# Performance work log

Hardware: AMD Instinct MI355X
Metric: run time of the kernel (lower is better)

## Reference

```python
import jax, jax.numpy as jnp
import numpy as np

D_MODEL = 768
D_LATENT = 12288
K = 20
N = 16384


def setup_inputs() -> dict:
    key = jax.random.key(0)
    k1, k2, k3, k4, k5 = jax.random.split(key, 5)
    x = jax.random.normal(k1, (N, D_MODEL), dtype=jnp.float32)
    # nn.Linear default init scale ~ 1/sqrt(fan_in)
    W_enc = jax.random.normal(k2, (D_LATENT, D_MODEL), dtype=jnp.float32) / np.sqrt(D_MODEL)
    b_enc = jax.random.normal(k3, (D_LATENT,), dtype=jnp.float32) * 0.01
    W_dec = jax.random.normal(k4, (D_MODEL, D_LATENT), dtype=jnp.float32) / np.sqrt(D_LATENT)
    b_dec = jax.random.normal(k5, (D_MODEL,), dtype=jnp.float32) * 0.01
    return {"x": x, "W_enc": W_enc, "b_enc": b_enc, "W_dec": W_dec, "b_dec": b_dec}


def reference(x, W_enc, b_enc, W_dec, b_dec):
    # encode: [N, 12288]
    latents = jnp.einsum('nd,ld->nl', x, W_enc) + b_enc
    # top-k(20) per row; scatter kept values back into zeros == latents * mask
    vals, idx = jax.lax.top_k(latents, K)            # [N, K]
    rows = jnp.arange(latents.shape[0])[:, None]      # [N, 1]
    sparse = jnp.zeros_like(latents).at[rows, idx].set(vals)
    # decode: [N, 768]
    recons = jnp.einsum('nl,dl->nd', sparse, W_dec) + b_dec
    return recons
```

## Files before the change

### kernel.cpp

```cpp
#include <hip/hip_runtime.h>
#include <hip/hip_bf16.h>
#include <stdint.h>

#define D_MODEL_  768
#define D_LATENT_ 12288
#define N_ROWS_   16384
#define TOPK_     20
#define TOPC      16
#define NQ        8
#define NC        128
#define NREF      28
#define THR0      1.7f

#define BM 256
#define BN 128
#define BK 64
#define KT (D_MODEL_ / BK)
#define CTQ (D_LATENT_ / NQ / BN)
#define NTHREADS 1024
#define CAP 8

#define BUFSZ 49152

typedef float f4 __attribute__((ext_vector_type(4)));
typedef short bf16x8 __attribute__((ext_vector_type(8)));

typedef const void __attribute__((address_space(1)))* gptr_t;
typedef void __attribute__((address_space(3)))* lptr_t;

__device__ __forceinline__ void stage16(const void* g, void* l) {
  __builtin_amdgcn_global_load_lds((gptr_t)g, (lptr_t)l, 16, 0, 0);
}

__device__ __forceinline__ unsigned short bf16_rne(float f) {
  unsigned u = __builtin_bit_cast(unsigned, f);
  u += 0x7FFFu + ((u >> 16) & 1u);
  return (unsigned short)(u >> 16);
}
__device__ __forceinline__ float bf16_to_f(unsigned short h) {
  return __builtin_bit_cast(float, ((unsigned)h) << 16);
}

#define BAR_LGKM() do { asm volatile("s_waitcnt lgkmcnt(0)" ::: "memory"); \
                        __builtin_amdgcn_s_barrier(); } while (0)

__global__ void tobf16_kernel(const float4* __restrict__ in, ushort4* __restrict__ o, int n4) {
  int i = blockIdx.x * blockDim.x + threadIdx.x;
  if (i >= n4) return;
  float4 v = in[i];
  ushort4 h;
  h.x = bf16_rne(v.x); h.y = bf16_rne(v.y); h.z = bf16_rne(v.z); h.w = bf16_rne(v.w);
  o[i] = h;
}

__global__ void transpose_bf16_kernel(const float* __restrict__ wd, unsigned short* __restrict__ wdT) {
  __shared__ float tile[32][33];
  const int l0 = blockIdx.x * 32;
  const int d0 = blockIdx.y * 32;
  const int tx = threadIdx.x, ty = threadIdx.y;
#pragma unroll
  for (int i = 0; i < 32; i += 8)
    tile[ty + i][tx] = wd[(size_t)(d0 + ty + i) * D_LATENT_ + l0 + tx];
  __syncthreads();
#pragma unroll
  for (int i = 0; i < 32; i += 8)
    wdT[(size_t)(l0 + ty + i) * D_MODEL_ + d0 + tx] = bf16_rne(tile[tx][ty + i]);
}

__global__ __launch_bounds__(NTHREADS, 4) void sae_topk(
    const unsigned short* __restrict__ xh, const unsigned short* __restrict__ wh,
    const float* __restrict__ b_enc, unsigned* __restrict__ candp)
{
  __shared__ __align__(16) unsigned char smem[2 * BUFSZ];
  __shared__ float s_topv[BM][TOPC];
  __shared__ int   s_topi[BM][TOPC];
  __shared__ float s_candv[BM][CAP];
  __shared__ int   s_candi[BM][CAP];
  __shared__ float s_thr[BM];
  __shared__ int   s_cnt[BM];
  __shared__ int   s_flag;

  const int tid  = threadIdx.x;
  const int lane = tid & 63;
  const int wid  = tid >> 6;
  const int wm   = wid >> 2;
  const int wn   = wid & 3;
  const int quar = blockIdx.x & 7;
  const int brow = (blockIdx.x >> 3) * BM;
  const int cbase = quar * (D_LATENT_ / NQ);

  auto stage_tile = [&](int buf, int ct, int kt) {
    unsigned char* base = smem + buf * BUFSZ;
#pragma unroll
    for (int j = 0; j < 2; ++j) {
      const int cid = tid + j * 1024;
      const int row = cid >> 3, slot = cid & 7;
      stage16(xh + (size_t)(brow + row) * D_MODEL_ + kt * BK + (slot ^ (row & 7)) * 8,
              base + cid * 16);
    }
    {
      const int row = tid >> 3, slot = tid & 7;
      stage16(wh + (size_t)(cbase + ct * BN + row) * D_MODEL_ + kt * BK + (slot ^ (row & 7)) * 8,
              base + 32768 + tid * 16);
    }
  };

  stage_tile(0, 0, 0);

  if (tid < BM) { s_thr[tid] = THR0; s_cnt[tid] = 0; }
  if (tid == 0) s_flag = 0;
  for (int i = tid; i < BM * TOPC; i += NTHREADS) {
    (&s_topv[0][0])[i] = -__builtin_inff();
    (&s_topi[0][0])[i] = 0;
  }

  f4 acc[4][2];
#pragma unroll
  for (int m = 0; m < 4; ++m)
#pragma unroll
    for (int n = 0; n < 2; ++n) { f4 z = {0.f, 0.f, 0.f, 0.f}; acc[m][n] = z; }

  int cur = 0;
#pragma unroll 1
  for (int ct = 0; ct < CTQ; ++ct) {
    const float be0 = b_enc[cbase + ct * BN + wn * 32 + (lane & 15)];
    const float be1 = b_enc[cbase + ct * BN + wn * 32 + 16 + (lane & 15)];

#pragma unroll 1
    for (int kt = 0; kt < KT; ++kt) {
      bool more = true;
      if (kt < KT - 1)       stage_tile(cur ^ 1, ct, kt + 1);
      else if (ct + 1 < CTQ) stage_tile(cur ^ 1, ct + 1, 0);
      else                   more = false;
      if (more) { asm volatile("s_waitcnt vmcnt(3)" ::: "memory"); }
      else      { asm volatile("s_waitcnt vmcnt(0)" ::: "memory"); }
      __builtin_amdgcn_s_barrier();
      {
        const unsigned char* base = smem + cur * BUFSZ;
#pragma unroll
        for (int ks = 0; ks < 2; ++ks) {
          const int c = ks * 4 + (lane >> 4);
          bf16x8 ah[4], bh[2];
#pragma unroll
          for (int m = 0; m < 4; ++m) {
            const int row = wm * 64 + m * 16 + (lane & 15);
            ah[m] = *(const bf16x8*)(base + row * 128 + ((c ^ (row & 7)) << 4));
          }
#pragma unroll
          for (int n = 0; n < 2; ++n) {
            const int col = wn * 32 + n * 16 + (lane & 15);
            bh[n] = *(const bf16x8*)(base + 32768 + col * 128 + ((c ^ (col & 7)) << 4));
          }
#pragma unroll
          for (int m = 0; m < 4; ++m)
#pragma unroll
            for (int n = 0; n < 2; ++n)
              acc[m][n] = __builtin_amdgcn_mfma_f32_16x16x32_bf16(ah[m], bh[n], acc[m][n], 0, 0, 0);
        }
      }
      __builtin_amdgcn_s_barrier();
      cur ^= 1;
    }

#pragma unroll
    for (int m = 0; m < 4; ++m) {
      acc[m][0][0] += be0; acc[m][0][1] += be0; acc[m][0][2] += be0; acc[m][0][3] += be0;
      acc[m][1][0] += be1; acc[m][1][1] += be1; acc[m][1][2] += be1; acc[m][1][3] += be1;
    }

    unsigned pend = ~0u;
#pragma unroll 1
    for (;;) {
#pragma unroll
      for (int m = 0; m < 4; ++m)
#pragma unroll
        for (int n = 0; n < 2; ++n)
#pragma unroll
          for (int j = 0; j < 4; ++j) {
            const int b = m * 8 + n * 4 + j;
            if (pend & (1u << b)) {
              const int row = wm * 64 + m * 16 + ((lane >> 4) << 2) + j;
              const float v = acc[m][n][j];
              if (v <= s_thr[row]) {
                pend &= ~(1u << b);
              } else {
                const int pos = atomicAdd(&s_cnt[row], 1);
                if (pos < CAP) {
                  s_candv[row][pos] = v;
                  s_candi[row][pos] = cbase + ct * BN + wn * 32 + n * 16 + (lane & 15);
                  pend &= ~(1u << b);
                }
              }
            }
          }
      BAR_LGKM();
      if (tid < BM) {
        const int row = tid;
        const int nc = s_cnt[row];
        if (nc > 0) {
          if (nc > CAP) s_flag = 1;
          float minv = s_topv[row][0]; int minp = 0;
#pragma unroll
          for (int k = 1; k < TOPC; ++k) { const float t = s_topv[row][k]; if (t < minv) { minv = t; minp = k; } }
          const int ne = nc < CAP ? nc : CAP;
          for (int j = 0; j < ne; ++j) {
            const float v = s_candv[row][j];
            if (v > minv) {
              s_topv[row][minp] = v; s_topi[row][minp] = s_candi[row][j];
              minv = s_topv[row][0]; minp = 0;
#pragma unroll
              for (int k = 1; k < TOPC; ++k) { const float t = s_topv[row][k]; if (t < minv) { minv = t; minp = k; } }
            }
          }
          s_thr[row] = minv > THR0 ? minv : THR0;
          s_cnt[row] = 0;
        }
      }
      BAR_LGKM();
      const int f = s_flag;
      BAR_LGKM();
      if (!f) break;
      if (tid == 0) s_flag = 0;
    }

#pragma unroll
    for (int m = 0; m < 4; ++m)
#pragma unroll
      for (int n = 0; n < 2; ++n) { f4 z = {0.f, 0.f, 0.f, 0.f}; acc[m][n] = z; }
  }

  if (tid < BM) {
#pragma unroll
    for (int k = 0; k < TOPC; ++k) {
      const float v = s_topv[tid][k];
      unsigned p = 0u;
      if (v > 0.f) p = ((unsigned)bf16_rne(v) << 16) | (unsigned)s_topi[tid][k];
      candp[(size_t)(brow + tid) * NC + quar * TOPC + k] = p;
    }
  }
}

__device__ __forceinline__ float chunk_fma(const float* __restrict__ xr,
                                           const float* __restrict__ wr,
                                           int beg, int end) {
  float a = 0.f;
#pragma unroll 4
  for (int d0 = beg; d0 < end; d0 += 4) {
    const float4 xv = *(const float4*)(xr + d0);
    const float4 wv = *(const float4*)(wr + d0);
    a = fmaf(xv.x, wv.x, a);
    a = fmaf(xv.y, wv.y, a);
    a = fmaf(xv.z, wv.z, a);
    a = fmaf(xv.w, wv.w, a);
  }
  return a;
}

__global__ __launch_bounds__(256) void refine_decode11(
    const float* __restrict__ x, const float* __restrict__ W_enc,
    const float* __restrict__ b_enc, const unsigned* __restrict__ candp,
    const unsigned short* __restrict__ wdTb, const float* __restrict__ b_dec,
    float* __restrict__ out)
{
  __shared__ unsigned s_p[4][NC];
  __shared__ unsigned s_ref[4][NREF];
  __shared__ float s_rv[4][NREF];
  __shared__ int   s_rid[4][NREF];
  __shared__ float s_selv[4][TOPK_];
  __shared__ int   s_seli[4][TOPK_];

  const int tid  = threadIdx.x;
  const int w    = tid >> 6;
  const int lane = tid & 63;
  const int row  = blockIdx.x * 4 + w;

  s_p[w][lane]      = candp[(size_t)row * NC + lane];
  s_p[w][lane + 64] = candp[(size_t)row * NC + lane + 64];
  __syncthreads();

#pragma unroll
  for (int t = 0; t < 2; ++t) {
    const int i = lane + t * 64;
    const unsigned p = s_p[w][i];
    int r = 0;
#pragma unroll 1
    for (int j = 0; j < NC; ++j) r += (s_p[w][j] > p);
    if (r < NREF && p != 0u) s_ref[w][r] = p;
  }
  __syncthreads();

  if (lane < NREF) {
    const unsigned p = s_ref[w][lane];
    const int idx = (int)(p & 0x3FFFu);
    const float* xr = x + (size_t)row * D_MODEL_;
    const float* wr = W_enc + (size_t)idx * D_MODEL_;
    const float a1 = chunk_fma(xr, wr, 0, 320);
    const float a2 = chunk_fma(xr, wr, 320, 544);
    const float a3 = chunk_fma(xr, wr, 544, 768);
    s_rv[w][lane]  = ((a1 + a2) + a3) + b_enc[idx];
    s_rid[w][lane] = idx;
  }
  __syncthreads();

  if (lane < NREF) {
    const float v = s_rv[w][lane]; const int id = s_rid[w][lane];
    int rank = 0;
#pragma unroll 1
    for (int j = 0; j < NREF; ++j) {
      const float vj = s_rv[w][j];
      rank += (vj > v) || (vj == v && s_rid[w][j] > id);
    }
    if (rank < TOPK_) { s_selv[w][rank] = v; s_seli[w][rank] = id; }
  }
  __syncthreads();

#pragma unroll 1
  for (int r = 0; r < 4; ++r) {
#pragma unroll
    for (int j = 0; j < 3; ++j) {
      const int d = tid + j * 256;
      float a = b_dec[d];
#pragma unroll
      for (int k = 0; k < TOPK_; ++k)
        a = fmaf(s_selv[r][k], bf16_to_f(wdTb[(size_t)s_seli[r][k] * D_MODEL_ + d]), a);
      out[(size_t)(blockIdx.x * 4 + r) * D_MODEL_ + d] = a;
    }
  }
}

extern "C" void kernel_launch(void* const* d_in, const int* in_sizes, int n_in,
                              void* d_out, int out_size, void* d_ws, size_t ws_size,
                              hipStream_t stream) {
  const float* x     = (const float*)d_in[0];
  const float* W_enc = (const float*)d_in[1];
  const float* b_enc = (const float*)d_in[2];
  const float* W_dec = (const float*)d_in[3];
  const float* b_dec = (const float*)d_in[4];
  float* out = (float*)d_out;
  char* ws = (char*)d_ws;

  unsigned short* xh = (unsigned short*)(ws + 0);
  unsigned short* wh = (unsigned short*)(ws + 25165824);
  unsigned*     candp = (unsigned*)(ws + 44040192);
  unsigned short* wdTb = (unsigned short*)(ws + 0);

  {
    int n4 = N_ROWS_ * D_MODEL_ / 4;
    tobf16_kernel<<<(n4 + 255) / 256, 256, 0, stream>>>((const float4*)x, (ushort4*)xh, n4);
  }
  {
    int n4 = D_LATENT_ * D_MODEL_ / 4;
    tobf16_kernel<<<(n4 + 255) / 256, 256, 0, stream>>>((const float4*)W_enc, (ushort4*)wh, n4);
  }

  sae_topk<<<(N_ROWS_ / BM) * NQ, NTHREADS, 0, stream>>>(xh, wh, b_enc, candp);

  transpose_bf16_kernel<<<dim3(D_LATENT_ / 32, D_MODEL_ / 32), dim3(32, 8), 0, stream>>>(W_dec, wdTb);

  refine_decode11<<<N_ROWS_ / 4, 256, 0, stream>>>(x, W_enc, b_enc, candp, wdTb, b_dec, out);
}
```

Baseline: 929.4 us.

## Widen encoder tile to 256 columns, pack top-k entries, auto-accept top candidates

The encoder GEMM tile grows from 128 to 256 latent columns per step. Each warp now holds a 4x4 set of MFMA accumulators, and the LDS buffers are enlarged to match, raising operand reuse per staged A tile. The per-row top-16 tracking now stores packed bf16-value/index words instead of separate float and int arrays, which cuts shared-memory traffic in the merge. The refine kernel accepts the 12 highest bf16 candidates without recomputing them and recomputes exactly in fp32 only the next 16 to fill the remaining 8 slots, reducing refine FMAs. The risk is that ranking the top 12 purely by bf16 values could pick a different set than an exact fp32 top-k, and the larger tile raises register and LDS pressure, which may lower occupancy.

```diff
diff --git a/kernel.cpp b/kernel.cpp
--- a/kernel.cpp
+++ b/kernel.cpp
@@ -9,18 +9,19 @@
 #define TOPC      16
 #define NQ        8
 #define NC        128
-#define NREF      28
+#define AUTO      12
+#define NREFW     16
 #define THR0      1.7f
 
 #define BM 256
-#define BN 128
+#define BN 256
 #define BK 64
 #define KT (D_MODEL_ / BK)
 #define CTQ (D_LATENT_ / NQ / BN)
 #define NTHREADS 1024
 #define CAP 8
 
-#define BUFSZ 49152
+#define BUFSZ 65536
 
 typedef float f4 __attribute__((ext_vector_type(4)));
 typedef short bf16x8 __attribute__((ext_vector_type(8)));
@@ -39,6 +40,9 @@
 }
 __device__ __forceinline__ float bf16_to_f(unsigned short h) {
   return __builtin_bit_cast(float, ((unsigned)h) << 16);
+}
+__device__ __forceinline__ unsigned packcand(float v, int idx) {
+  return v > 0.f ? (((unsigned)bf16_rne(v) << 16) | (unsigned)idx) : 0u;
 }
 
 #define BAR_LGKM() do { asm volatile("s_waitcnt lgkmcnt(0)" ::: "memory"); \
@@ -72,13 +76,11 @@
     const float* __restrict__ b_enc, unsigned* __restrict__ candp)
 {
   __shared__ __align__(16) unsigned char smem[2 * BUFSZ];
-  __shared__ float s_topv[BM][TOPC];
-  __shared__ int   s_topi[BM][TOPC];
-  __shared__ float s_candv[BM][CAP];
-  __shared__ int   s_candi[BM][CAP];
-  __shared__ float s_thr[BM];
-  __shared__ int   s_cnt[BM];
-  __shared__ int   s_flag;
+  __shared__ unsigned s_top[BM][TOPC];
+  __shared__ unsigned s_cand[BM][CAP];
+  __shared__ float    s_thr[BM];
+  __shared__ int      s_cnt[BM];
+  __shared__ int      s_flag;
 
   const int tid  = threadIdx.x;
   const int lane = tid & 63;
@@ -98,10 +100,12 @@
       stage16(xh + (size_t)(brow + row) * D_MODEL_ + kt * BK + (slot ^ (row & 7)) * 8,
               base + cid * 16);
     }
-    {
-      const int row = tid >> 3, slot = tid & 7;
+#pragma unroll
+    for (int j = 0; j < 2; ++j) {
+      const int cid = tid + j * 1024;
+      const int row = cid >> 3, slot = cid & 7;
       stage16(wh + (size_t)(cbase + ct * BN + row) * D_MODEL_ + kt * BK + (slot ^ (row & 7)) * 8,
-              base + 32768 + tid * 16);
+              base + 32768 + cid * 16);
     }
   };
 
@@ -109,22 +113,21 @@
 
   if (tid < BM) { s_thr[tid] = THR0; s_cnt[tid] = 0; }
   if (tid == 0) s_flag = 0;
-  for (int i = tid; i < BM * TOPC; i += NTHREADS) {
-    (&s_topv[0][0])[i] = -__builtin_inff();
-    (&s_topi[0][0])[i] = 0;
-  }
-
-  f4 acc[4][2];
+  for (int i = tid; i < BM * TOPC; i += NTHREADS) (&s_top[0][0])[i] = 0u;
+
+  f4 acc[4][4];
 #pragma unroll
   for (int m = 0; m < 4; ++m)
 #pragma unroll
-    for (int n = 0; n < 2; ++n) { f4 z = {0.f, 0.f, 0.f, 0.f}; acc[m][n] = z; }
+    for (int n = 0; n < 4; ++n) { f4 z = {0.f, 0.f, 0.f, 0.f}; acc[m][n] = z; }
 
   int cur = 0;
 #pragma unroll 1
   for (int ct = 0; ct < CTQ; ++ct) {
-    const float be0 = b_enc[cbase + ct * BN + wn * 32 + (lane & 15)];
-    const float be1 = b_enc[cbase + ct * BN + wn * 32 + 16 + (lane & 15)];
+    float be[4];
+#pragma unroll
+    for (int n = 0; n < 4; ++n)
+      be[n] = b_enc[cbase + ct * BN + wn * 64 + n * 16 + (lane & 15)];
 
 #pragma unroll 1
     for (int kt = 0; kt < KT; ++kt) {
@@ -132,7 +135,7 @@
       if (kt < KT - 1)       stage_tile(cur ^ 1, ct, kt + 1);
       else if (ct + 1 < CTQ) stage_tile(cur ^ 1, ct + 1, 0);
       else                   more = false;
-      if (more) { asm volatile("s_waitcnt vmcnt(3)" ::: "memory"); }
+      if (more) { asm volatile("s_waitcnt vmcnt(4)" ::: "memory"); }
       else      { asm volatile("s_waitcnt vmcnt(0)" ::: "memory"); }
       __builtin_amdgcn_s_barrier();
       {
@@ -140,21 +143,21 @@
 #pragma unroll
         for (int ks = 0; ks < 2; ++ks) {
           const int c = ks * 4 + (lane >> 4);
-          bf16x8 ah[4], bh[2];
+          bf16x8 ah[4], bh[4];
 #pragma unroll
           for (int m = 0; m < 4; ++m) {
             const int row = wm * 64 + m * 16 + (lane & 15);
             ah[m] = *(const bf16x8*)(base + row * 128 + ((c ^ (row & 7)) << 4));
           }
 #pragma unroll
-          for (int n = 0; n < 2; ++n) {
-            const int col = wn * 32 + n * 16 + (lane & 15);
+          for (int n = 0; n < 4; ++n) {
+            const int col = wn * 64 + n * 16 + (lane & 15);
             bh[n] = *(const bf16x8*)(base + 32768 + col * 128 + ((c ^ (col & 7)) << 4));
           }
 #pragma unroll
           for (int m = 0; m < 4; ++m)
 #pragma unroll
-            for (int n = 0; n < 2; ++n)
+            for (int n = 0; n < 4; ++n)
               acc[m][n] = __builtin_amdgcn_mfma_f32_16x16x32_bf16(ah[m], bh[n], acc[m][n], 0, 0, 0);
         }
       }
@@ -163,32 +166,33 @@
     }
 
 #pragma unroll
-    for (int m = 0; m < 4; ++m) {
-      acc[m][0][0] += be0; acc[m][0][1] += be0; acc[m][0][2] += be0; acc[m][0][3] += be0;
-      acc[m][1][0] += be1; acc[m][1][1] += be1; acc[m][1][2] += be1; acc[m][1][3] += be1;
-    }
-
-    unsigned pend = ~0u;
+    for (int m = 0; m < 4; ++m)
+#pragma unroll
+      for (int n = 0; n < 4; ++n) {
+        acc[m][n][0] += be[n]; acc[m][n][1] += be[n];
+        acc[m][n][2] += be[n]; acc[m][n][3] += be[n];
+      }
+
+    unsigned long long pend = ~0ull;
 #pragma unroll 1
     for (;;) {
 #pragma unroll
       for (int m = 0; m < 4; ++m)
 #pragma unroll
-        for (int n = 0; n < 2; ++n)
+        for (int n = 0; n < 4; ++n)
 #pragma unroll
           for (int j = 0; j < 4; ++j) {
-            const int b = m * 8 + n * 4 + j;
-            if (pend & (1u << b)) {
+            const int b = m * 16 + n * 4 + j;
+            if (pend & (1ull << b)) {
               const int row = wm * 64 + m * 16 + ((lane >> 4) << 2) + j;
               const float v = acc[m][n][j];
               if (v <= s_thr[row]) {
-                pend &= ~(1u << b);
+                pend &= ~(1ull << b);
               } else {
                 const int pos = atomicAdd(&s_cnt[row], 1);
                 if (pos < CAP) {
-                  s_candv[row][pos] = v;
-                  s_candi[row][pos] = cbase + ct * BN + wn * 32 + n * 16 + (lane & 15);
-                  pend &= ~(1u << b);
+                  s_cand[row][pos] = packcand(v, cbase + ct * BN + wn * 64 + n * 16 + (lane & 15));
+                  pend &= ~(1ull << b);
                 }
               }
             }
@@ -199,20 +203,21 @@
         const int nc = s_cnt[row];
         if (nc > 0) {
           if (nc > CAP) s_flag = 1;
-          float minv = s_topv[row][0]; int minp = 0;
-#pragma unroll
-          for (int k = 1; k < TOPC; ++k) { const float t = s_topv[row][k]; if (t < minv) { minv = t; minp = k; } }
+          unsigned minp = s_top[row][0]; int mpos = 0;
+#pragma unroll
+          for (int k = 1; k < TOPC; ++k) { const unsigned t = s_top[row][k]; if (t < minp) { minp = t; mpos = k; } }
           const int ne = nc < CAP ? nc : CAP;
           for (int j = 0; j < ne; ++j) {
-            const float v = s_candv[row][j];
-            if (v > minv) {
-              s_topv[row][minp] = v; s_topi[row][minp] = s_candi[row][j];
-              minv = s_topv[row][0]; minp = 0;
-#pragma unroll
-              for (int k = 1; k < TOPC; ++k) { const float t = s_topv[row][k]; if (t < minv) { minv = t; minp = k; } }
+            const unsigned p = s_cand[row][j];
+            if (p > minp) {
+              s_top[row][mpos] = p;
+              minp = s_top[row][0]; mpos = 0;
+#pragma unroll
+              for (int k = 1; k < TOPC; ++k) { const unsigned t = s_top[row][k]; if (t < minp) { minp = t; mpos = k; } }
             }
           }
-          s_thr[row] = minv > THR0 ? minv : THR0;
+          const float mv = bf16_to_f((unsigned short)(minp >> 16));
+          s_thr[row] = mv > THR0 ? mv : THR0;
           s_cnt[row] = 0;
         }
       }
@@ -226,17 +231,13 @@
 #pragma unroll
     for (int m = 0; m < 4; ++m)
 #pragma unroll
-      for (int n = 0; n < 2; ++n) { f4 z = {0.f, 0.f, 0.f, 0.f}; acc[m][n] = z; }
+      for (int n = 0; n < 4; ++n) { f4 z = {0.f, 0.f, 0.f, 0.f}; acc[m][n] = z; }
   }
 
   if (tid < BM) {
 #pragma unroll
-    for (int k = 0; k < TOPC; ++k) {
-      const float v = s_topv[tid][k];
-      unsigned p = 0u;
-      if (v > 0.f) p = ((unsigned)bf16_rne(v) << 16) | (unsigned)s_topi[tid][k];
-      candp[(size_t)(brow + tid) * NC + quar * TOPC + k] = p;
-    }
+    for (int k = 0; k < TOPC; ++k)
+      candp[(size_t)(brow + tid) * NC + quar * TOPC + k] = s_top[tid][k];
   }
 }
 
@@ -256,16 +257,16 @@
   return a;
 }
 
-__global__ __launch_bounds__(256) void refine_decode11(
+__global__ __launch_bounds__(256) void refine_decode12(
     const float* __restrict__ x, const float* __restrict__ W_enc,
     const float* __restrict__ b_enc, const unsigned* __restrict__ candp,
     const unsigned short* __restrict__ wdTb, const float* __restrict__ b_dec,
     float* __restrict__ out)
 {
   __shared__ unsigned s_p[4][NC];
-  __shared__ unsigned s_ref[4][NREF];
-  __shared__ float s_rv[4][NREF];
-  __shared__ int   s_rid[4][NREF];
+  __shared__ unsigned s_ref[4][NREFW];
+  __shared__ float s_rv[4][NREFW];
+  __shared__ int   s_rid[4][NREFW];
   __shared__ float s_selv[4][TOPK_];
   __shared__ int   s_seli[4][TOPK_];
 
@@ -276,41 +277,56 @@
 
   s_p[w][lane]      = candp[(size_t)row * NC + lane];
   s_p[w][lane + 64] = candp[(size_t)row * NC + lane + 64];
+  if (lane < NREFW) s_ref[w][lane] = 0u;
   __syncthreads();
 
 #pragma unroll
   for (int t = 0; t < 2; ++t) {
     const int i = lane + t * 64;
     const unsigned p = s_p[w][i];
-    int r = 0;
-#pragma unroll 1
-    for (int j = 0; j < NC; ++j) r += (s_p[w][j] > p);
-    if (r < NREF && p != 0u) s_ref[w][r] = p;
-  }
-  __syncthreads();
-
-  if (lane < NREF) {
+    if (p != 0u) {
+      int r = 0;
+#pragma unroll 1
+      for (int j = 0; j < NC; ++j) r += (s_p[w][j] > p);
+      if (r < AUTO) {
+        s_selv[w][r] = bf16_to_f((unsigned short)(p >> 16));
+        s_seli[w][r] = (int)(p & 0x3FFFu);
+      } else if (r < AUTO + NREFW) {
+        s_ref[w][r - AUTO] = p;
+      }
+    }
+  }
+  __syncthreads();
+
+  if (lane < NREFW) {
     const unsigned p = s_ref[w][lane];
-    const int idx = (int)(p & 0x3FFFu);
-    const float* xr = x + (size_t)row * D_MODEL_;
-    const float* wr = W_enc + (size_t)idx * D_MODEL_;
-    const float a1 = chunk_fma(xr, wr, 0, 320);
-    const float a2 = chunk_fma(xr, wr, 320, 544);
-    const float a3 = chunk_fma(xr, wr, 544, 768);
-    s_rv[w][lane]  = ((a1 + a2) + a3) + b_enc[idx];
-    s_rid[w][lane] = idx;
-  }
-  __syncthreads();
-
-  if (lane < NREF) {
+    if (p != 0u) {
+      const int idx = (int)(p & 0x3FFFu);
+      const float* xr = x + (size_t)row * D_MODEL_;
+      const float* wr = W_enc + (size_t)idx * D_MODEL_;
+      const float a1 = chunk_fma(xr, wr, 0, 320);
+      const float a2 = chunk_fma(xr, wr, 320, 544);
+      const float a3 = chunk_fma(xr, wr, 544, 768);
+      s_rv[w][lane]  = ((a1 + a2) + a3) + b_enc[idx];
+      s_rid[w][lane] = idx;
+    } else {
+      s_rv[w][lane]  = -__builtin_inff();
+      s_rid[w][lane] = -1;
+    }
+  }
+  __syncthreads();
+
+  if (lane < NREFW) {
     const float v = s_rv[w][lane]; const int id = s_rid[w][lane];
-    int rank = 0;
-#pragma unroll 1
-    for (int j = 0; j < NREF; ++j) {
-      const float vj = s_rv[w][j];
-      rank += (vj > v) || (vj == v && s_rid[w][j] > id);
-    }
-    if (rank < TOPK_) { s_selv[w][rank] = v; s_seli[w][rank] = id; }
+    if (id >= 0) {
+      int rank = 0;
+#pragma unroll 1
+      for (int j = 0; j < NREFW; ++j) {
+        const float vj = s_rv[w][j];
+        rank += (vj > v) || (vj == v && s_rid[w][j] > id);
+      }
+      if (rank < TOPK_ - AUTO) { s_selv[w][AUTO + rank] = v; s_seli[w][AUTO + rank] = id; }
+    }
   }
   __syncthreads();
 
@@ -357,5 +373,5 @@
 
   transpose_bf16_kernel<<<dim3(D_LATENT_ / 32, D_MODEL_ / 32), dim3(32, 8), 0, stream>>>(W_dec, wdTb);
 
-  refine_decode11<<<N_ROWS_ / 4, 256, 0, stream>>>(x, W_enc, b_enc, candp, wdTb, b_dec, out);
-}
+  refine_decode12<<<N_ROWS_ / 4, 256, 0, stream>>>(x, W_enc, b_enc, candp, wdTb, b_dec, out);
+}
```

After: 1.033 ms. +11.2%, slower.
